# Optimization experiments

Measured on AMD Instinct MI355X. Metric: run time of the kernel, lower is better.

The kernel has to match this reference:

```python
import jax, jax.numpy as jnp
import numpy as np

N, E = 20000, 320000
CIN = 128; H = 128
EDGE_DIM = 16; SDIM = 3; KS = 3
K = KS ** SDIM          # 27 kernel weight matrices
S = 2 ** SDIM           # 8 non-zero B-spline taps per edge (degree-1)
MLP_HID = 2 * SDIM


def _glorot(key, shape, fan_in):
    return jax.random.normal(key, shape, dtype=jnp.float32) / np.sqrt(fan_in)


def setup_inputs() -> dict:
    key = jax.random.key(0)
    ks = jax.random.split(key, 16)
    inp = {
        "x": jax.random.normal(ks[0], (N, CIN), dtype=jnp.float32),
        "edge_index": jax.random.randint(ks[1], (2, E), 0, N, dtype=jnp.int64),
        "edge_attr": jax.random.normal(ks[2], (E, EDGE_DIM), dtype=jnp.float32),
        # edge preprocessor MLP
        "Wp1": _glorot(ks[3], (EDGE_DIM, MLP_HID), EDGE_DIM),
        "bp1": jnp.zeros((MLP_HID,), jnp.float32),
        "Wp2": _glorot(ks[4], (MLP_HID, SDIM), MLP_HID),
        "bp2": jnp.zeros((SDIM,), jnp.float32),
    }
    cins = [CIN, H, H]
    for l in range(3):
        inp[f"W{l}"] = _glorot(ks[5 + 3 * l], (K, cins[l], H), cins[l] * 2)
        inp[f"Wr{l}"] = _glorot(ks[6 + 3 * l], (cins[l], H), cins[l])
        inp[f"b{l}"] = jnp.zeros((H,), jnp.float32)
    return inp


def spline_basis(u):
    """Degree-1 open B-spline basis. u: [E, SDIM] in [0,1].
    Returns (weights [E,S], flat kernel indices [E,S])."""
    v = u * (KS - 1)
    lo = jnp.clip(jnp.floor(v), 0, KS - 2)
    frac = v - lo                      # [E, SDIM]
    lo = lo.astype(jnp.int32)
    ws, idxs = [], []
    for s in range(S):
        w = jnp.ones(u.shape[0], dtype=u.dtype)
        idx = jnp.zeros(u.shape[0], dtype=jnp.int32)
        stride = 1
        for d in range(SDIM):
            bit = (s >> d) & 1
            w = w * (frac[:, d] if bit else (1.0 - frac[:, d]))
            idx = idx + (lo[:, d] + bit) * stride
            stride *= KS
        ws.append(w); idxs.append(idx)
    return jnp.stack(ws, 1), jnp.stack(idxs, 1)


def spline_conv(x, src, dst, bw, bidx, W, Wr, b):
    """SplineConv with sum aggregation, root weight and bias."""
    cin = x.shape[1]
    x_src = x[src]                              # [E, Cin] gather
    T = jnp.zeros((N * K, cin), dtype=x.dtype)  # per-(node, kernel-idx) accumulator
    for s in range(S):                          # fixed small tap count
        seg = dst * K + bidx[:, s]              # [E]
        T = T + jax.ops.segment_sum(bw[:, s, None] * x_src, seg, num_segments=N * K)
    T = T.reshape(N, K, cin)
    return jnp.einsum('nki,kio->no', T, W) + x @ Wr + b


def reference(x, edge_index, edge_attr, Wp1, bp1, Wp2, bp2,
              W0, Wr0, b0, W1, Wr1, b1, W2, Wr2, b2):
    src = edge_index[0].astype(jnp.int32)
    dst = edge_index[1].astype(jnp.int32)
    # edge preprocessor MLP + sigmoid -> pseudo coords in (0,1)
    u = jax.nn.sigmoid(jax.nn.relu(edge_attr @ Wp1 + bp1) @ Wp2 + bp2)
    bw, bidx = spline_basis(u)
    h = spline_conv(x, src, dst, bw, bidx, W0, Wr0, b0)
    h = jax.nn.relu(h)  # dropout: eval mode (identity)
    h = spline_conv(h, src, dst, bw, bidx, W1, Wr1, b1)
    h = jax.nn.relu(h)
    h = spline_conv(h, src, dst, bw, bidx, W2, Wr2, b2)
    return h
```

## Files before the change

### kernel.cpp

```cpp
#include <hip/hip_runtime.h>
#include <hip/hip_bf16.h>
#include <hip/hip_fp16.h>

#define N_NODES 20000
#define E_EDGES 320000
#define CIN 128
#define HDIM 128
#define EDGE_DIM 16
#define SDIM 3
#define KS 3
#define KK 27
#define NB 28
#define KSTEPS 112
#define TLD (KK * 128)
#define RLD 32
#define EPAD 8
#define MLP_HID 6

typedef __attribute__((ext_vector_type(8))) short v8s;
typedef __attribute__((ext_vector_type(4))) float v4f;
typedef unsigned short ush;

static __device__ __forceinline__ short f2bf(float v) {
    unsigned u = __float_as_uint(v);
    unsigned r = (u + 0x7fffu + ((u >> 16) & 1u)) >> 16;
    return (short)r;
}
static __device__ __forceinline__ float bf2f_lo(unsigned u) {
    return __uint_as_float(u << 16);
}
static __device__ __forceinline__ float bf2f_hi(unsigned u) {
    return __uint_as_float(u & 0xffff0000u);
}
static __device__ __forceinline__ unsigned pack2bf(float a, float b) {
    return ((unsigned)(ush)f2bf(a)) | (((unsigned)(ush)f2bf(b)) << 16);
}

__global__ void detect_kernel(const unsigned int* __restrict__ e, int* __restrict__ flag) {
    __shared__ int s_nz;
    if (threadIdx.x == 0) s_nz = 0;
    __syncthreads();
    unsigned int v = e[threadIdx.x * 2 + 1];
    if (v != 0) atomicAdd(&s_nz, 1);
    __syncthreads();
    if (threadIdx.x == 0) *flag = (s_nz > 0) ? 1 : 0;
}

__global__ void decode_edges(const void* __restrict__ eraw, const int* __restrict__ flag,
                             int* __restrict__ e32, int n) {
    int i = blockIdx.x * blockDim.x + threadIdx.x;
    if (i >= n) return;
    if (*flag) e32[i] = ((const int*)eraw)[i];
    else       e32[i] = (int)(((const long long*)eraw)[i]);
}

__global__ void edge_basis(const float* __restrict__ ea,
                           const float* __restrict__ Wp1, const float* __restrict__ bp1,
                           const float* __restrict__ Wp2, const float* __restrict__ bp2,
                           float4* __restrict__ fb) {
    __shared__ float sW1[EDGE_DIM * MLP_HID];
    __shared__ float sb1[MLP_HID];
    __shared__ float sW2[MLP_HID * SDIM];
    __shared__ float sb2[SDIM];
    int t = threadIdx.x;
    if (t < EDGE_DIM * MLP_HID) sW1[t] = Wp1[t];
    if (t < MLP_HID)            sb1[t] = bp1[t];
    if (t < MLP_HID * SDIM)     sW2[t] = Wp2[t];
    if (t < SDIM)               sb2[t] = bp2[t];
    __syncthreads();
    int e = blockIdx.x * blockDim.x + t;
    if (e >= E_EDGES) return;

    float a[EDGE_DIM];
#pragma unroll
    for (int i = 0; i < EDGE_DIM; i++) a[i] = ea[(long)e * EDGE_DIM + i];

    float hid[MLP_HID];
#pragma unroll
    for (int j = 0; j < MLP_HID; j++) {
        float s = sb1[j];
#pragma unroll
        for (int i = 0; i < EDGE_DIM; i++) s += a[i] * sW1[i * MLP_HID + j];
        hid[j] = fmaxf(s, 0.f);
    }

    float fr[SDIM];
    unsigned lp = 0;
#pragma unroll
    for (int d = 0; d < SDIM; d++) {
        float s = sb2[d];
#pragma unroll
        for (int j = 0; j < MLP_HID; j++) s += hid[j] * sW2[j * SDIM + d];
        float u = 1.f / (1.f + expf(-s));
        float v = u * (float)(KS - 1);
        float l = floorf(v);
        l = fminf(fmaxf(l, 0.f), (float)(KS - 2));
        fr[d] = v - l;
        lp |= ((unsigned)(int)l) << (8 * d);
    }
    float4 o;
    o.x = fr[0]; o.y = fr[1]; o.z = fr[2]; o.w = __uint_as_float(lp);
    fb[e] = o;
}

__global__ void zero_int(int* __restrict__ p, int n) {
    int i = blockIdx.x * blockDim.x + threadIdx.x;
    if (i < n) p[i] = 0;
}

__global__ void hist_kernel(const int* __restrict__ dst, int* __restrict__ hist) {
    int e = blockIdx.x * blockDim.x + threadIdx.x;
    if (e >= E_EDGES) return;
    atomicAdd(&hist[dst[e]], 1);
}

__global__ void scan_blk(const int* __restrict__ hist, int* __restrict__ rowptr,
                         int* __restrict__ bsum, int B) {
    __shared__ int sh[256];
    int i = blockIdx.x * 256 + threadIdx.x;
    int v = (i < B) ? hist[i] : 0;
    sh[threadIdx.x] = v;
    __syncthreads();
    for (int off = 1; off < 256; off <<= 1) {
        int t = (threadIdx.x >= off) ? sh[threadIdx.x - off] : 0;
        __syncthreads();
        sh[threadIdx.x] += t;
        __syncthreads();
    }
    if (i < B) rowptr[i] = sh[threadIdx.x] - v;
    if (threadIdx.x == 255) bsum[blockIdx.x] = sh[255];
}

__global__ void scan_top(int* __restrict__ bsum, int nb) {
    __shared__ int sh[256];
    int v = (threadIdx.x < nb) ? bsum[threadIdx.x] : 0;
    sh[threadIdx.x] = v;
    __syncthreads();
    for (int off = 1; off < 256; off <<= 1) {
        int t = (threadIdx.x >= off) ? sh[threadIdx.x - off] : 0;
        __syncthreads();
        sh[threadIdx.x] += t;
        __syncthreads();
    }
    if (threadIdx.x < nb) bsum[threadIdx.x] = sh[threadIdx.x] - v;
}

__global__ void scan_add(int* __restrict__ rowptr, const int* __restrict__ bsum, int B) {
    int i = blockIdx.x * 256 + threadIdx.x;
    if (i < B) rowptr[i] += bsum[blockIdx.x];
    if (i == 0) rowptr[B] = E_EDGES;
}

__global__ void perm_kernel(const int* __restrict__ dst,
                            const int* __restrict__ rowptr, int* __restrict__ cursor,
                            int* __restrict__ eperm) {
    int e = blockIdx.x * blockDim.x + threadIdx.x;
    if (e >= E_EDGES) return;
    int bin = dst[e];
    int pos = rowptr[bin] + atomicAdd(&cursor[bin], 1);
    eperm[pos] = e;
}

__global__ void pack_rec(const int* __restrict__ eperm, const int* __restrict__ src,
                         const float4* __restrict__ fb, float* __restrict__ rec) {
    int j = blockIdx.x * blockDim.x + threadIdx.x;
    if (j >= E_EDGES + EPAD) return;
    float out[RLD];
#pragma unroll
    for (int q = 0; q < RLD; q++) out[q] = 0.f;
    if (j < E_EDGES) {
        int e = eperm[j];
        out[0] = __int_as_float(src[e]);
        float4 f = fb[e];
        unsigned lp = __float_as_uint(f.w);
        float fr[3] = {f.x, f.y, f.z};
        float t[3][3];
#pragma unroll
        for (int d = 0; d < 3; d++) {
            int lo = (lp >> (8 * d)) & 255;
            float fd = fr[d];
#pragma unroll
            for (int q = 0; q < 3; q++)
                t[d][q] = (q == lo) ? (1.f - fd) : (q == lo + 1) ? fd : 0.f;
        }
#pragma unroll
        for (int k2 = 0; k2 < 3; k2++)
#pragma unroll
            for (int k1 = 0; k1 < 3; k1++)
#pragma unroll
                for (int k0 = 0; k0 < 3; k0++)
                    out[4 + k2 * 9 + k1 * 3 + k0] = t[0][k0] * t[1][k1] * t[2][k2];
    }
    float* op = rec + (size_t)j * RLD;
#pragma unroll
    for (int q = 0; q < RLD / 4; q++) *(float4*)(op + 4 * q) = *(float4*)(out + 4 * q);
}

__global__ void packW3_kernel(const float* __restrict__ W0, const float* __restrict__ Wr0,
                              const float* __restrict__ W1, const float* __restrict__ Wr1,
                              const float* __restrict__ W2, const float* __restrict__ Wr2,
                              short* __restrict__ hi) {
    int gid = blockIdx.x * blockDim.x + threadIdx.x;
    if (gid >= 3 * NB * 4 * 8 * 64) return;
    int lane = gid & 63;
    int nt = (gid >> 6) & 7;
    int ks = (gid >> 9) & 3;
    int kb2 = gid >> 11;
    int layer = kb2 / NB;
    int kb = kb2 - layer * NB;
    const float* W  = (layer == 0) ? W0  : (layer == 1) ? W1  : W2;
    const float* Wr = (layer == 0) ? Wr0 : (layer == 1) ? Wr1 : Wr2;
    int i0 = ks * 32 + ((lane >> 4) & 3) * 8;
    int o = nt * 16 + (lane & 15);
    const float* src = (kb < KK) ? (W + (long)kb * 16384 + (long)i0 * 128 + o)
                                 : (Wr + (long)i0 * 128 + o);
    long off = ((long)(((size_t)layer * NB + kb) * 4 + ks) * 8 + nt) * 64 * 8
             + (long)lane * 8;
#pragma unroll
    for (int j = 0; j < 8; j++) {
        float v = src[(long)j * 128];
        hi[off + j] = f2bf(v);
    }
}

__global__ void conv_xb(const float* __restrict__ x, ush* __restrict__ xb) {
    int i = blockIdx.x * blockDim.x + threadIdx.x;
    if (i >= N_NODES * CIN / 4) return;
    float4 v = ((const float4*)x)[i];
    uint2 d;
    d.x = pack2bf(v.x, v.y);
    d.y = pack2bf(v.z, v.w);
    ((uint2*)xb)[i] = d;
}

__global__ __launch_bounds__(64) void accumT_kernel(
    const ush* __restrict__ act, const int* __restrict__ rowptr,
    const float* __restrict__ rec, ush* __restrict__ T, int n0)
{
    __shared__ float lb[2][256];
    int lane = threadIdx.x;
    int n = n0 + blockIdx.x;
    int jb = rowptr[n], je = rowptr[n + 1];
    int d = je - jb;

    float acc[KK][2];
#pragma unroll
    for (int k = 0; k < KK; k++) { acc[k][0] = 0.f; acc[k][1] = 0.f; }

    const ush* actl = act + lane * 2;

    if (d > 0) {
        int nb = (d + 7) >> 3;
        const float4* rb = (const float4*)rec + (size_t)jb * 8;

        float4 g = rb[lane];
        *(float4*)(&lb[0][lane * 4]) = g;
        if (nb > 1) g = rb[(size_t)64 + lane];

        for (int b = 0; b < nb; ++b) {
            int slot = b & 1;
            if (b + 1 < nb) *(float4*)(&lb[slot ^ 1][lane * 4]) = g;
            if (b + 2 < nb) g = rb[(size_t)(b + 2) * 64 + lane];

            int sidx[8];
#pragma unroll
            for (int e = 0; e < 8; e++)
                sidx[e] = __float_as_int(lb[slot][e * 32]);
            unsigned xa[8];
#pragma unroll
            for (int e = 0; e < 8; e++)
                xa[e] = *(const unsigned*)(actl + (size_t)sidx[e] * 128);

            int rem = d - (b << 3);
#pragma unroll
            for (int e = 0; e < 8; e++) {
                if (e < rem) {
                    float w[28];
#pragma unroll
                    for (int q = 0; q < 7; q++)
                        *(float4*)(w + 4 * q) =
                            *(const float4*)(&lb[slot][e * 32 + 4 + 4 * q]);
                    float x0 = bf2f_lo(xa[e]), x1 = bf2f_hi(xa[e]);
#pragma unroll
                    for (int k = 0; k < KK; k++) {
                        acc[k][0] += w[k] * x0;
                        acc[k][1] += w[k] * x1;
                    }
                }
            }
        }
    }

    ush* tp = T + (size_t)(n - n0) * TLD + lane * 2;
#pragma unroll
    for (int k = 0; k < KK; k++) {
        *(unsigned*)(tp + (size_t)k * 128) = pack2bf(acc[k][0], acc[k][1]);
    }
}

__global__ __launch_bounds__(1024) void gemm2_kernel(
    const ush* __restrict__ T, const ush* __restrict__ act,
    const short* __restrict__ Wh, const float* __restrict__ bias,
    ush* __restrict__ actout, float* __restrict__ fout,
    int n0, int relu)
{
    __shared__ float S[1024][17];
    int lane = threadIdx.x & 63;
    int wave = threadIdx.x >> 6;
    int mtr = blockIdx.x;

    v4f acc[8];
#pragma unroll
    for (int nt = 0; nt < 8; nt++) acc[nt] = (v4f){0.f, 0.f, 0.f, 0.f};

    int r15 = lane & 15;
    int sub = (lane >> 4) & 3;
    int arow = mtr * 16 + r15;
    const ush* tp = T + (size_t)arow * TLD + sub * 8;
    const ush* ap = act + (size_t)(n0 + arow) * 128 + sub * 8;

    int ks0 = wave * (KSTEPS / 16);
#pragma unroll
    for (int i = 0; i < KSTEPS / 16; i++) {
        int ks = ks0 + i;
        v8s a = (ks < KK * 4) ? *(const v8s*)(tp + ks * 32)
                              : *(const v8s*)(ap + (ks - KK * 4) * 32);
        const short* wb = Wh + (size_t)ks * 4096 + (size_t)lane * 8;
#pragma unroll
        for (int nt = 0; nt < 8; nt++) {
            v8s b = *(const v8s*)(wb + (size_t)nt * 512);
            acc[nt] = __builtin_amdgcn_mfma_f32_16x16x32_bf16(a, b, acc[nt], 0, 0, 0);
        }
    }

    int r  = threadIdx.x >> 6;
    int cl = threadIdx.x & 63;
    int row = n0 + mtr * 16 + r;
#pragma unroll
    for (int p = 0; p < 2; p++) {
        __syncthreads();
#pragma unroll
        for (int q = 0; q < 16; q++)
            S[threadIdx.x][q] = acc[p * 4 + (q >> 2)][q & 3];
        __syncthreads();
        int c = p * 64 + cl;
        int ln  = (cl & 15) + 16 * (r >> 2);
        int idx = (cl >> 4) * 4 + (r & 3);
        float s = 0.f;
#pragma unroll
        for (int w = 0; w < 16; w++) s += S[w * 64 + ln][idx];
        s += bias[c];
        if (relu) s = fmaxf(s, 0.f);
        if (actout) {
            actout[(size_t)row * 128 + c] = (ush)f2bf(s);
        } else {
            fout[(size_t)row * 128 + c] = s;
        }
    }
}

extern "C" void kernel_launch(void* const* d_in, const int* in_sizes, int n_in,
                              void* d_out, int out_size, void* d_ws, size_t ws_size,
                              hipStream_t stream) {
    const float* x   = (const float*)d_in[0];
    const void*  eix = d_in[1];
    const float* ea  = (const float*)d_in[2];
    const float* Wp1 = (const float*)d_in[3];
    const float* bp1 = (const float*)d_in[4];
    const float* Wp2 = (const float*)d_in[5];
    const float* bp2 = (const float*)d_in[6];
    const float* W[3]  = {(const float*)d_in[7],  (const float*)d_in[10], (const float*)d_in[13]};
    const float* Wr[3] = {(const float*)d_in[8],  (const float*)d_in[11], (const float*)d_in[14]};
    const float* b[3]  = {(const float*)d_in[9],  (const float*)d_in[12], (const float*)d_in[15]};
    float* out = (float*)d_out;

    char* ws = (char*)d_ws;
    size_t off = 0;
    auto walloc = [&](size_t bytes) -> void* {
        void* p = ws + off;
        off = (off + bytes + 255) & ~(size_t)255;
        return p;
    };
    int*    flag    = (int*)   walloc(sizeof(int));
    int*    e32     = (int*)   walloc(sizeof(int) * 2 * E_EDGES);
    float4* fb      = (float4*)walloc(sizeof(float4) * (size_t)E_EDGES);
    int*    eperm   = (int*)   walloc(sizeof(int) * E_EDGES);
    float*  rec     = (float*) walloc(sizeof(float) * (size_t)(E_EDGES + EPAD) * RLD);
    int*    histcur = (int*)   walloc(sizeof(int) * (size_t)N_NODES * 2);
    int*    rowptr  = (int*)   walloc(sizeof(int) * (N_NODES + 1));
    int*    bsum    = (int*)   walloc(sizeof(int) * 256);
    ush*    xb      = (ush*)   walloc(sizeof(ush) * (size_t)N_NODES * 128);
    ush*    a1      = (ush*)   walloc(sizeof(ush) * (size_t)N_NODES * 128);
    ush*    a2      = (ush*)   walloc(sizeof(ush) * (size_t)N_NODES * 128);
    short*  Wh3     = (short*) walloc(sizeof(short) * (size_t)3 * NB * 128 * 128);

    int chunk_n = 2000;
    {
        const int cand[4] = {20000, 10000, 4000, 2000};
        for (int i = 0; i < 4; i++) {
            size_t need = (size_t)cand[i] * TLD * sizeof(ush);
            chunk_n = cand[i];
            if (off + need <= ws_size) break;
        }
    }
    ush* T = (ush*)walloc((size_t)chunk_n * TLD * sizeof(ush));

    int* srcv = e32;
    int* dstv = e32 + E_EDGES;
    int* hist   = histcur;
    int* cursor = histcur + N_NODES;

    detect_kernel<<<1, 1024, 0, stream>>>((const unsigned int*)eix, flag);
    decode_edges<<<(2 * E_EDGES + 255) / 256, 256, 0, stream>>>(eix, flag, e32, 2 * E_EDGES);
    edge_basis<<<(E_EDGES + 255) / 256, 256, 0, stream>>>(ea, Wp1, bp1, Wp2, bp2, fb);

    const int NBLK = (N_NODES + 255) / 256;
    zero_int<<<(N_NODES * 2 + 255) / 256, 256, 0, stream>>>(histcur, N_NODES * 2);
    hist_kernel<<<(E_EDGES + 255) / 256, 256, 0, stream>>>(dstv, hist);
    scan_blk<<<NBLK, 256, 0, stream>>>(hist, rowptr, bsum, N_NODES);
    scan_top<<<1, 256, 0, stream>>>(bsum, NBLK);
    scan_add<<<NBLK, 256, 0, stream>>>(rowptr, bsum, N_NODES);
    perm_kernel<<<(E_EDGES + 255) / 256, 256, 0, stream>>>(dstv, rowptr, cursor, eperm);
    pack_rec<<<(E_EDGES + EPAD + 255) / 256, 256, 0, stream>>>(eperm, srcv, fb, rec);

    packW3_kernel<<<(3 * NB * 4 * 8 * 64 + 255) / 256, 256, 0, stream>>>(
        W[0], Wr[0], W[1], Wr[1], W[2], Wr[2], Wh3);
    conv_xb<<<(N_NODES * CIN / 4 + 255) / 256, 256, 0, stream>>>(x, xb);

    const ush* actin = xb;
    for (int l = 0; l < 3; l++) {
        const short* Wh = Wh3 + (size_t)l * NB * 128 * 128;
        ush* actout = (l == 0) ? a1 : (l == 1) ? a2 : nullptr;
        for (int n0 = 0; n0 < N_NODES; n0 += chunk_n) {
            int cn = (n0 + chunk_n <= N_NODES) ? chunk_n : (N_NODES - n0);
            int nmt = cn / 16;
            accumT_kernel<<<cn, 64, 0, stream>>>(actin, rowptr, rec, T, n0);
            gemm2_kernel<<<nmt, 1024, 0, stream>>>(
                T, actin, Wh, b[l], actout, (l == 2) ? out : nullptr,
                n0, (l < 2) ? 1 : 0);
        }
        if (l == 0) actin = a1; else if (l == 1) actin = a2;
    }
}
```

Baseline: 526.8 us.

## Pack four nodes per accumT block and two M-tiles per GEMM block

The accumulation kernel now runs four waves per block, each handling its own destination node with a private shared-memory staging buffer, which cuts the block count and per-block launch overhead. The GEMM kernel now computes two 16-row M-tiles per block, so each loaded weight fragment feeds two MFMAs and weight traffic from L2 is halved. This doubles accumulator registers in the GEMM, which may reduce occupancy, and the edge padding grows to 16 to cover the larger record reads.

Result: no change. 518.7 us (-1.5%).

```diff
diff --git a/kernel.cpp b/kernel.cpp
--- a/kernel.cpp
+++ b/kernel.cpp
@@ -14,7 +14,7 @@
 #define KSTEPS 112
 #define TLD (KK * 128)
 #define RLD 32
-#define EPAD 8
+#define EPAD 16
 #define MLP_HID 6
 
 typedef __attribute__((ext_vector_type(8))) short v8s;
@@ -233,13 +233,15 @@
     ((uint2*)xb)[i] = d;
 }
 
-__global__ __launch_bounds__(64) void accumT_kernel(
+__global__ __launch_bounds__(256) void accumT_kernel(
     const ush* __restrict__ act, const int* __restrict__ rowptr,
-    const float* __restrict__ rec, ush* __restrict__ T, int n0)
+    const float* __restrict__ rec, ush* __restrict__ T, int n0, int nmax)
 {
-    __shared__ float lb[2][256];
-    int lane = threadIdx.x;
-    int n = n0 + blockIdx.x;
+    __shared__ float lb[4][2][256];
+    int lane = threadIdx.x & 63;
+    int wave = threadIdx.x >> 6;
+    int n = n0 + blockIdx.x * 4 + wave;
+    if (n >= nmax) return;
     int jb = rowptr[n], je = rowptr[n + 1];
     int d = je - jb;
 
@@ -254,18 +256,18 @@
         const float4* rb = (const float4*)rec + (size_t)jb * 8;
 
         float4 g = rb[lane];
-        *(float4*)(&lb[0][lane * 4]) = g;
+        *(float4*)(&lb[wave][0][lane * 4]) = g;
         if (nb > 1) g = rb[(size_t)64 + lane];
 
         for (int b = 0; b < nb; ++b) {
             int slot = b & 1;
-            if (b + 1 < nb) *(float4*)(&lb[slot ^ 1][lane * 4]) = g;
+            if (b + 1 < nb) *(float4*)(&lb[wave][slot ^ 1][lane * 4]) = g;
             if (b + 2 < nb) g = rb[(size_t)(b + 2) * 64 + lane];
 
             int sidx[8];
 #pragma unroll
             for (int e = 0; e < 8; e++)
-                sidx[e] = __float_as_int(lb[slot][e * 32]);
+                sidx[e] = __float_as_int(lb[wave][slot][e * 32]);
             unsigned xa[8];
 #pragma unroll
             for (int e = 0; e < 8; e++)
@@ -279,7 +281,7 @@
 #pragma unroll
                     for (int q = 0; q < 7; q++)
                         *(float4*)(w + 4 * q) =
-                            *(const float4*)(&lb[slot][e * 32 + 4 + 4 * q]);
+                            *(const float4*)(&lb[wave][slot][e * 32 + 4 + 4 * q]);
                     float x0 = bf2f_lo(xa[e]), x1 = bf2f_hi(xa[e]);
 #pragma unroll
                     for (int k = 0; k < KK; k++) {
@@ -302,59 +304,73 @@
     const ush* __restrict__ T, const ush* __restrict__ act,
     const short* __restrict__ Wh, const float* __restrict__ bias,
     ush* __restrict__ actout, float* __restrict__ fout,
-    int n0, int relu)
+    int n0, int nmt, int relu)
 {
     __shared__ float S[1024][17];
     int lane = threadIdx.x & 63;
     int wave = threadIdx.x >> 6;
-    int mtr = blockIdx.x;
-
-    v4f acc[8];
-#pragma unroll
-    for (int nt = 0; nt < 8; nt++) acc[nt] = (v4f){0.f, 0.f, 0.f, 0.f};
+    int mtr0 = blockIdx.x * 2;
+    int mv = (nmt - mtr0 >= 2) ? 2 : 1;
+
+    v4f acc[2][8];
+#pragma unroll
+    for (int m = 0; m < 2; m++)
+#pragma unroll
+        for (int nt = 0; nt < 8; nt++) acc[m][nt] = (v4f){0.f, 0.f, 0.f, 0.f};
 
     int r15 = lane & 15;
     int sub = (lane >> 4) & 3;
-    int arow = mtr * 16 + r15;
-    const ush* tp = T + (size_t)arow * TLD + sub * 8;
-    const ush* ap = act + (size_t)(n0 + arow) * 128 + sub * 8;
+    int arow0 = mtr0 * 16 + r15;
+    int arow1 = arow0 + ((mv > 1) ? 16 : 0);
+    const ush* tp0 = T + (size_t)arow0 * TLD + sub * 8;
+    const ush* tp1 = T + (size_t)arow1 * TLD + sub * 8;
+    const ush* ap0 = act + (size_t)(n0 + arow0) * 128 + sub * 8;
+    const ush* ap1 = act + (size_t)(n0 + arow1) * 128 + sub * 8;
 
     int ks0 = wave * (KSTEPS / 16);
 #pragma unroll
     for (int i = 0; i < KSTEPS / 16; i++) {
         int ks = ks0 + i;
-        v8s a = (ks < KK * 4) ? *(const v8s*)(tp + ks * 32)
-                              : *(const v8s*)(ap + (ks - KK * 4) * 32);
+        v8s a0 = (ks < KK * 4) ? *(const v8s*)(tp0 + ks * 32)
+                               : *(const v8s*)(ap0 + (ks - KK * 4) * 32);
+        v8s a1 = (ks < KK * 4) ? *(const v8s*)(tp1 + ks * 32)
+                               : *(const v8s*)(ap1 + (ks - KK * 4) * 32);
         const short* wb = Wh + (size_t)ks * 4096 + (size_t)lane * 8;
 #pragma unroll
         for (int nt = 0; nt < 8; nt++) {
             v8s b = *(const v8s*)(wb + (size_t)nt * 512);
-            acc[nt] = __builtin_amdgcn_mfma_f32_16x16x32_bf16(a, b, acc[nt], 0, 0, 0);
+            acc[0][nt] = __builtin_amdgcn_mfma_f32_16x16x32_bf16(a0, b, acc[0][nt], 0, 0, 0);
+            acc[1][nt] = __builtin_amdgcn_mfma_f32_16x16x32_bf16(a1, b, acc[1][nt], 0, 0, 0);
         }
     }
 
     int r  = threadIdx.x >> 6;
     int cl = threadIdx.x & 63;
-    int row = n0 + mtr * 16 + r;
-#pragma unroll
-    for (int p = 0; p < 2; p++) {
-        __syncthreads();
-#pragma unroll
-        for (int q = 0; q < 16; q++)
-            S[threadIdx.x][q] = acc[p * 4 + (q >> 2)][q & 3];
-        __syncthreads();
-        int c = p * 64 + cl;
-        int ln  = (cl & 15) + 16 * (r >> 2);
-        int idx = (cl >> 4) * 4 + (r & 3);
-        float s = 0.f;
-#pragma unroll
-        for (int w = 0; w < 16; w++) s += S[w * 64 + ln][idx];
-        s += bias[c];
-        if (relu) s = fmaxf(s, 0.f);
-        if (actout) {
-            actout[(size_t)row * 128 + c] = (ush)f2bf(s);
-        } else {
-            fout[(size_t)row * 128 + c] = s;
+#pragma unroll
+    for (int m = 0; m < 2; m++) {
+        int row = n0 + (mtr0 + m) * 16 + r;
+#pragma unroll
+        for (int p = 0; p < 2; p++) {
+            __syncthreads();
+#pragma unroll
+            for (int q = 0; q < 16; q++)
+                S[threadIdx.x][q] = acc[m][p * 4 + (q >> 2)][q & 3];
+            __syncthreads();
+            if (m < mv) {
+                int c = p * 64 + cl;
+                int ln  = (cl & 15) + 16 * (r >> 2);
+                int idx = (cl >> 4) * 4 + (r & 3);
+                float s = 0.f;
+#pragma unroll
+                for (int w = 0; w < 16; w++) s += S[w * 64 + ln][idx];
+                s += bias[c];
+                if (relu) s = fmaxf(s, 0.f);
+                if (actout) {
+                    actout[(size_t)row * 128 + c] = (ush)f2bf(s);
+                } else {
+                    fout[(size_t)row * 128 + c] = s;
+                }
+            }
         }
     }
 }
@@ -434,10 +450,11 @@
         for (int n0 = 0; n0 < N_NODES; n0 += chunk_n) {
             int cn = (n0 + chunk_n <= N_NODES) ? chunk_n : (N_NODES - n0);
             int nmt = cn / 16;
-            accumT_kernel<<<cn, 64, 0, stream>>>(actin, rowptr, rec, T, n0);
-            gemm2_kernel<<<nmt, 1024, 0, stream>>>(
+            accumT_kernel<<<(cn + 3) / 4, 256, 0, stream>>>(
+                actin, rowptr, rec, T, n0, n0 + cn);
+            gemm2_kernel<<<(nmt + 1) / 2, 1024, 0, stream>>>(
                 T, actin, Wh, b[l], actout, (l == 2) ? out : nullptr,
-                n0, (l < 2) ? 1 : 0);
+                n0, nmt, (l < 2) ? 1 : 0);
         }
         if (l == 0) actin = a1; else if (l == 1) actin = a2;
     }
```
